# Performance work log

Measured on AMD Instinct MI355X. Metric: run time of the kernel, lower is better.

## Reference

```python
import jax, jax.numpy as jnp
import numpy as np

B, N, D, H = 2, 2048, 1024, 16
DH = D // H
SCALE = DH ** -0.5

def setup_inputs() -> dict:
    key = jax.random.key(0)
    k1, k2, k3 = jax.random.split(key, 3)
    x = jax.random.normal(k1, (B, N, D), dtype=jnp.float32)
    W_qkv = jax.random.normal(k2, (3 * D, D), dtype=jnp.float32) * (D ** -0.5)
    W_out = jax.random.normal(k3, (D, D), dtype=jnp.float32) * (D ** -0.5)
    mask = jnp.tril(jnp.ones((N, N), dtype=jnp.int32))  # causal mask; 0 -> -inf
    return {"x": x, "mask": mask, "W_qkv": W_qkv, "W_out": W_out}

def reference(x, mask, W_qkv, W_out):
    b, n, d = x.shape
    qkv = x @ W_qkv.T                                   # [B,N,3D]
    qkv = qkv.reshape(b, n, 3, H, DH).transpose(2, 0, 3, 1, 4)  # [3,B,H,N,DH]
    q, k, v = qkv[0], qkv[1], qkv[2]
    attn = jnp.einsum('bhqd,bhkd->bhqk', q, k) * SCALE  # [B,H,N,N]
    attn = jnp.where(mask == 0, -jnp.inf, attn)
    attn = jax.nn.softmax(attn, axis=-1)
    out = jnp.einsum('bhqk,bhkd->bhqd', attn, v)        # [B,H,N,DH]
    out = out.transpose(0, 2, 1, 3).reshape(b, n, d)    # [B,N,D]
    return out @ W_out.T
```

## Files before the change

### kernel.cpp

```cpp
#include <hip/hip_runtime.h>
#include <hip/hip_bf16.h>


typedef __hip_bfloat16 bf16;
typedef short bf16x8 __attribute__((ext_vector_type(8)));
typedef short bf16x4 __attribute__((ext_vector_type(4)));
typedef float f32x4 __attribute__((ext_vector_type(4)));

#define QSCALE 0.1803368801111204f

typedef __attribute__((address_space(3))) unsigned int lds_u32;
typedef const __attribute__((address_space(1))) unsigned int glob_u32;

__device__ __forceinline__ void glds16(const void* g, void* l) {
    __builtin_amdgcn_global_load_lds((glob_u32*)g, (lds_u32*)l, 16, 0, 0);
}

__device__ __forceinline__ short f2bf(float f) {
    __hip_bfloat16 h = __float2bfloat16(f);
    return *reinterpret_cast<short*>(&h);
}

__device__ __forceinline__ unsigned pack_bf16(float a, float b) {
    unsigned au = __builtin_bit_cast(unsigned, a) + 0x8000u;
    unsigned bu = __builtin_bit_cast(unsigned, b) + 0x8000u;
    return __builtin_amdgcn_perm(bu, au, 0x07060302u);
}

__global__ void cast4(const float* __restrict__ src, bf16* __restrict__ dst, int n4) {
    int i = blockIdx.x * blockDim.x + threadIdx.x;
    if (i < n4) {
        float4 f = reinterpret_cast<const float4*>(src)[i];
        short4 s;
        s.x = f2bf(f.x); s.y = f2bf(f.y); s.z = f2bf(f.z); s.w = f2bf(f.w);
        reinterpret_cast<short4*>(dst)[i] = s;
    }
}

template<int EPI>
__global__ __launch_bounds__(256)
void gemm128(const bf16* __restrict__ A, const bf16* __restrict__ Bt,
             float* __restrict__ Cf,
             bf16* __restrict__ qp, bf16* __restrict__ kp, bf16* __restrict__ vp,
             int K, int Ncols) {
    __shared__ alignas(16) short As[2][4096];
    __shared__ alignas(16) short Bs[2][4096];

    const int tid = threadIdx.x;
    const int wave = tid >> 6, lane = tid & 63;
    const int quad = lane >> 4, l16 = lane & 15;
    const int wm = wave >> 1, wn = wave & 1;
    const int m0 = blockIdx.x * 128;
    const int n0 = blockIdx.y * 128;

    f32x4 acc[4][4] = {};

    const int srow = tid >> 2;
    const int skk  = (((tid & 3) ^ ((tid >> 3) & 3))) * 8;
    const bf16* Ag = A  + (size_t)(m0 + srow) * K + skk;
    const bf16* Bg = Bt + (size_t)(n0 + srow) * K + skk;
    const size_t rowskip = (size_t)64 * K;
    short* Asl = &As[0][0] + tid * 8;
    short* Bsl = &Bs[0][0] + tid * 8;

    const int xk = (quad ^ ((l16 >> 1) & 3)) * 8;
    const int arow = wm * 64 + l16;
    const int brow = wn * 64 + l16;

    const int KI = K >> 5;
    glds16(Ag, Asl);
    glds16(Ag + rowskip, Asl + 2048);
    glds16(Bg, Bsl);
    glds16(Bg + rowskip, Bsl + 2048);
    __syncthreads();

    int buf = 0;
    for (int ki = 0; ki < KI; ++ki) {
        if (ki + 1 < KI) {
            const bf16* ag = Ag + (ki + 1) * 32;
            const bf16* bg = Bg + (ki + 1) * 32;
            short* ad = Asl + (buf ^ 1) * 4096;
            short* bd = Bsl + (buf ^ 1) * 4096;
            glds16(ag, ad);
            glds16(ag + rowskip, ad + 2048);
            glds16(bg, bd);
            glds16(bg + rowskip, bd + 2048);
        }
        const short* ab = &As[buf][0];
        const short* bb = &Bs[buf][0];
        bf16x8 af[4], bf[4];
        #pragma unroll
        for (int mt = 0; mt < 4; ++mt)
            af[mt] = *reinterpret_cast<const bf16x8*>(ab + (arow + mt * 16) * 32 + xk);
        #pragma unroll
        for (int nt = 0; nt < 4; ++nt)
            bf[nt] = *reinterpret_cast<const bf16x8*>(bb + (brow + nt * 16) * 32 + xk);
        #pragma unroll
        for (int mt = 0; mt < 4; ++mt)
            #pragma unroll
            for (int nt = 0; nt < 4; ++nt)
                acc[mt][nt] = __builtin_amdgcn_mfma_f32_16x16x32_bf16(
                    af[mt], bf[nt], acc[mt][nt], 0, 0, 0);
        __syncthreads();
        buf ^= 1;
    }

    #pragma unroll
    for (int mt = 0; mt < 4; ++mt) {
        #pragma unroll
        for (int nt = 0; nt < 4; ++nt) {
            #pragma unroll
            for (int r = 0; r < 4; ++r) {
                int gm = m0 + wm * 64 + mt * 16 + quad * 4 + r;
                int gn = n0 + wn * 64 + nt * 16 + l16;
                float val = acc[mt][nt][r];
                if (EPI == 0) {
                    int sel = gn >> 10, rem = gn & 1023;
                    int h = rem >> 6, dh = rem & 63;
                    int b = gm >> 11, nq = gm & 2047;
                    if (sel == 0) val *= QSCALE;
                    bf16* dst = (sel == 0) ? qp : ((sel == 1) ? kp : vp);
                    dst[((((size_t)b * 16 + h) * 2048) + nq) * 64 + dh] = __float2bfloat16(val);
                } else {
                    Cf[(size_t)gm * Ncols + gn] = val;
                }
            }
        }
    }
}

__global__ __launch_bounds__(256)
void flash_attn(const bf16* __restrict__ Q, const bf16* __restrict__ K,
                const bf16* __restrict__ V, bf16* __restrict__ O) {
    __shared__ alignas(16) short Ks[2][64][72];
    __shared__ alignas(16) short Vt[2][64][68];

    const int tid = threadIdx.x;
    const int wave = tid >> 6, lane = tid & 63;
    const int quad = lane >> 4, l16 = lane & 15;
    const int bh = blockIdx.x;
    const int yy = blockIdx.y;
    const int qt = (yy < 8) ? yy : (15 - (yy & 7));
    const int Q0 = qt * 128;
    const float NEG_INF = -__builtin_inff();

    const bf16* Qb = Q + (size_t)bh * 2048 * 64;
    const bf16* Kb = K + (size_t)bh * 2048 * 64;
    const bf16* Vb = V + (size_t)bh * 2048 * 64;

    const int qrowA = Q0 + wave * 16 + l16;
    const int qrowB = qrowA + 64;
    const bf16x8 qfA0 = *reinterpret_cast<const bf16x8*>(Qb + (size_t)qrowA * 64 + quad * 8);
    const bf16x8 qfA1 = *reinterpret_cast<const bf16x8*>(Qb + (size_t)qrowA * 64 + 32 + quad * 8);
    const bf16x8 qfB0 = *reinterpret_cast<const bf16x8*>(Qb + (size_t)qrowB * 64 + quad * 8);
    const bf16x8 qfB1 = *reinterpret_cast<const bf16x8*>(Qb + (size_t)qrowB * 64 + 32 + quad * 8);

    float lA = 0.f, lB = 0.f;
    f32x4 oA[4] = {}, oB[4] = {};

    const int krow = tid >> 2;
    const int kcol = (tid & 3) * 16;
    const int kb = (tid & 15) * 4;
    const int db = (tid >> 4) * 4;

    {
        bf16x8 a0 = *reinterpret_cast<const bf16x8*>(Kb + (size_t)krow * 64 + kcol);
        bf16x8 a1 = *reinterpret_cast<const bf16x8*>(Kb + (size_t)krow * 64 + kcol + 8);
        bf16x4 L0 = *reinterpret_cast<const bf16x4*>(Vb + (size_t)(kb + 0) * 64 + db);
        bf16x4 L1 = *reinterpret_cast<const bf16x4*>(Vb + (size_t)(kb + 1) * 64 + db);
        bf16x4 L2 = *reinterpret_cast<const bf16x4*>(Vb + (size_t)(kb + 2) * 64 + db);
        bf16x4 L3 = *reinterpret_cast<const bf16x4*>(Vb + (size_t)(kb + 3) * 64 + db);
        *reinterpret_cast<bf16x8*>(&Ks[0][krow][kcol]) = a0;
        *reinterpret_cast<bf16x8*>(&Ks[0][krow][kcol + 8]) = a1;
        #pragma unroll
        for (int j = 0; j < 4; ++j) {
            bf16x4 w; w[0] = L0[j]; w[1] = L1[j]; w[2] = L2[j]; w[3] = L3[j];
            *reinterpret_cast<bf16x4*>(&Vt[0][db + j][kb]) = w;
        }
    }
    __syncthreads();

    int buf = 0;
    for (int j0 = 0; j0 < Q0; j0 += 64) {
        const bf16* Kn = Kb + (size_t)(j0 + 64) * 64;
        const bf16* Vn = Vb + (size_t)(j0 + 64) * 64;
        bf16x8 nk0 = *reinterpret_cast<const bf16x8*>(Kn + (size_t)krow * 64 + kcol);
        bf16x8 nk1 = *reinterpret_cast<const bf16x8*>(Kn + (size_t)krow * 64 + kcol + 8);
        bf16x4 N0 = *reinterpret_cast<const bf16x4*>(Vn + (size_t)(kb + 0) * 64 + db);
        bf16x4 N1 = *reinterpret_cast<const bf16x4*>(Vn + (size_t)(kb + 1) * 64 + db);
        bf16x4 N2 = *reinterpret_cast<const bf16x4*>(Vn + (size_t)(kb + 2) * 64 + db);
        bf16x4 N3 = *reinterpret_cast<const bf16x4*>(Vn + (size_t)(kb + 3) * 64 + db);

        bf16x4 pkA[4], pkB[4];
        #pragma unroll
        for (int t = 0; t < 4; ++t) {
            bf16x8 k0 = *reinterpret_cast<const bf16x8*>(&Ks[buf][16 * t + l16][quad * 8]);
            bf16x8 k1 = *reinterpret_cast<const bf16x8*>(&Ks[buf][16 * t + l16][32 + quad * 8]);
            f32x4 sA = {}, sB = {};
            sA = __builtin_amdgcn_mfma_f32_16x16x32_bf16(k0, qfA0, sA, 0, 0, 0);
            sA = __builtin_amdgcn_mfma_f32_16x16x32_bf16(k1, qfA1, sA, 0, 0, 0);
            sB = __builtin_amdgcn_mfma_f32_16x16x32_bf16(k0, qfB0, sB, 0, 0, 0);
            sB = __builtin_amdgcn_mfma_f32_16x16x32_bf16(k1, qfB1, sB, 0, 0, 0);
            float a0 = __builtin_amdgcn_exp2f(sA[0]);
            float a1 = __builtin_amdgcn_exp2f(sA[1]);
            float a2 = __builtin_amdgcn_exp2f(sA[2]);
            float a3 = __builtin_amdgcn_exp2f(sA[3]);
            float b0 = __builtin_amdgcn_exp2f(sB[0]);
            float b1 = __builtin_amdgcn_exp2f(sB[1]);
            float b2 = __builtin_amdgcn_exp2f(sB[2]);
            float b3 = __builtin_amdgcn_exp2f(sB[3]);
            lA += (a0 + a1) + (a2 + a3);
            lB += (b0 + b1) + (b2 + b3);
            unsigned* pa = reinterpret_cast<unsigned*>(&pkA[t]);
            pa[0] = pack_bf16(a0, a1); pa[1] = pack_bf16(a2, a3);
            unsigned* pb = reinterpret_cast<unsigned*>(&pkB[t]);
            pb[0] = pack_bf16(b0, b1); pb[1] = pack_bf16(b2, b3);
        }

        #pragma unroll
        for (int t = 0; t < 4; ++t) {
            #pragma unroll
            for (int dt = 0; dt < 4; ++dt) {
                bf16x4 vf = *reinterpret_cast<const bf16x4*>(
                    &Vt[buf][dt * 16 + l16][t * 16 + quad * 4]);
                oA[dt] = __builtin_amdgcn_mfma_f32_16x16x16bf16_1k(vf, pkA[t], oA[dt], 0, 0, 0);
                oB[dt] = __builtin_amdgcn_mfma_f32_16x16x16bf16_1k(vf, pkB[t], oB[dt], 0, 0, 0);
            }
        }

        *reinterpret_cast<bf16x8*>(&Ks[buf ^ 1][krow][kcol]) = nk0;
        *reinterpret_cast<bf16x8*>(&Ks[buf ^ 1][krow][kcol + 8]) = nk1;
        #pragma unroll
        for (int j = 0; j < 4; ++j) {
            bf16x4 w; w[0] = N0[j]; w[1] = N1[j]; w[2] = N2[j]; w[3] = N3[j];
            *reinterpret_cast<bf16x4*>(&Vt[buf ^ 1][db + j][kb]) = w;
        }
        __syncthreads();
        buf ^= 1;
    }

    {
        const bf16* Kn = Kb + (size_t)(Q0 + 64) * 64;
        const bf16* Vn = Vb + (size_t)(Q0 + 64) * 64;
        bf16x8 nk0 = *reinterpret_cast<const bf16x8*>(Kn + (size_t)krow * 64 + kcol);
        bf16x8 nk1 = *reinterpret_cast<const bf16x8*>(Kn + (size_t)krow * 64 + kcol + 8);
        bf16x4 N0 = *reinterpret_cast<const bf16x4*>(Vn + (size_t)(kb + 0) * 64 + db);
        bf16x4 N1 = *reinterpret_cast<const bf16x4*>(Vn + (size_t)(kb + 1) * 64 + db);
        bf16x4 N2 = *reinterpret_cast<const bf16x4*>(Vn + (size_t)(kb + 2) * 64 + db);
        bf16x4 N3 = *reinterpret_cast<const bf16x4*>(Vn + (size_t)(kb + 3) * 64 + db);

        bf16x4 pkA[4], pkB[4];
        #pragma unroll
        for (int t = 0; t < 4; ++t) {
            bf16x8 k0 = *reinterpret_cast<const bf16x8*>(&Ks[buf][16 * t + l16][quad * 8]);
            bf16x8 k1 = *reinterpret_cast<const bf16x8*>(&Ks[buf][16 * t + l16][32 + quad * 8]);
            f32x4 sB = {};
            sB = __builtin_amdgcn_mfma_f32_16x16x32_bf16(k0, qfB0, sB, 0, 0, 0);
            sB = __builtin_amdgcn_mfma_f32_16x16x32_bf16(k1, qfB1, sB, 0, 0, 0);
            float b0 = __builtin_amdgcn_exp2f(sB[0]);
            float b1 = __builtin_amdgcn_exp2f(sB[1]);
            float b2 = __builtin_amdgcn_exp2f(sB[2]);
            float b3 = __builtin_amdgcn_exp2f(sB[3]);
            lB += (b0 + b1) + (b2 + b3);
            unsigned* pb = reinterpret_cast<unsigned*>(&pkB[t]);
            pb[0] = pack_bf16(b0, b1); pb[1] = pack_bf16(b2, b3);
            if (t <= wave) {
                f32x4 sA = {};
                sA = __builtin_amdgcn_mfma_f32_16x16x32_bf16(k0, qfA0, sA, 0, 0, 0);
                sA = __builtin_amdgcn_mfma_f32_16x16x32_bf16(k1, qfA1, sA, 0, 0, 0);
                if (t == wave) {
                    #pragma unroll
                    for (int r = 0; r < 4; ++r)
                        if (quad * 4 + r > l16) sA[r] = NEG_INF;
                }
                float a0 = __builtin_amdgcn_exp2f(sA[0]);
                float a1 = __builtin_amdgcn_exp2f(sA[1]);
                float a2 = __builtin_amdgcn_exp2f(sA[2]);
                float a3 = __builtin_amdgcn_exp2f(sA[3]);
                lA += (a0 + a1) + (a2 + a3);
                unsigned* pa = reinterpret_cast<unsigned*>(&pkA[t]);
                pa[0] = pack_bf16(a0, a1); pa[1] = pack_bf16(a2, a3);
            }
        }
        #pragma unroll
        for (int t = 0; t < 4; ++t) {
            #pragma unroll
            for (int dt = 0; dt < 4; ++dt) {
                bf16x4 vf = *reinterpret_cast<const bf16x4*>(
                    &Vt[buf][dt * 16 + l16][t * 16 + quad * 4]);
                oB[dt] = __builtin_amdgcn_mfma_f32_16x16x16bf16_1k(vf, pkB[t], oB[dt], 0, 0, 0);
                if (t <= wave)
                    oA[dt] = __builtin_amdgcn_mfma_f32_16x16x16bf16_1k(vf, pkA[t], oA[dt], 0, 0, 0);
            }
        }

        *reinterpret_cast<bf16x8*>(&Ks[buf ^ 1][krow][kcol]) = nk0;
        *reinterpret_cast<bf16x8*>(&Ks[buf ^ 1][krow][kcol + 8]) = nk1;
        #pragma unroll
        for (int j = 0; j < 4; ++j) {
            bf16x4 w; w[0] = N0[j]; w[1] = N1[j]; w[2] = N2[j]; w[3] = N3[j];
            *reinterpret_cast<bf16x4*>(&Vt[buf ^ 1][db + j][kb]) = w;
        }
        __syncthreads();
        buf ^= 1;
    }

    {
        bf16x4 pkB[4];
        #pragma unroll
        for (int t = 0; t < 4; ++t) {
            if (t <= wave) {
                bf16x8 k0 = *reinterpret_cast<const bf16x8*>(&Ks[buf][16 * t + l16][quad * 8]);
                bf16x8 k1 = *reinterpret_cast<const bf16x8*>(&Ks[buf][16 * t + l16][32 + quad * 8]);
                f32x4 sB = {};
                sB = __builtin_amdgcn_mfma_f32_16x16x32_bf16(k0, qfB0, sB, 0, 0, 0);
                sB = __builtin_amdgcn_mfma_f32_16x16x32_bf16(k1, qfB1, sB, 0, 0, 0);
                if (t == wave) {
                    #pragma unroll
                    for (int r = 0; r < 4; ++r)
                        if (quad * 4 + r > l16) sB[r] = NEG_INF;
                }
                float b0 = __builtin_amdgcn_exp2f(sB[0]);
                float b1 = __builtin_amdgcn_exp2f(sB[1]);
                float b2 = __builtin_amdgcn_exp2f(sB[2]);
                float b3 = __builtin_amdgcn_exp2f(sB[3]);
                lB += (b0 + b1) + (b2 + b3);
                unsigned* pb = reinterpret_cast<unsigned*>(&pkB[t]);
                pb[0] = pack_bf16(b0, b1); pb[1] = pack_bf16(b2, b3);
            }
        }
        #pragma unroll
        for (int t = 0; t < 4; ++t) {
            if (t <= wave) {
                #pragma unroll
                for (int dt = 0; dt < 4; ++dt) {
                    bf16x4 vf = *reinterpret_cast<const bf16x4*>(
                        &Vt[buf][dt * 16 + l16][t * 16 + quad * 4]);
                    oB[dt] = __builtin_amdgcn_mfma_f32_16x16x16bf16_1k(vf, pkB[t], oB[dt], 0, 0, 0);
                }
            }
        }
    }

    lA += __shfl_xor(lA, 16, 64);
    lA += __shfl_xor(lA, 32, 64);
    lB += __shfl_xor(lB, 16, 64);
    lB += __shfl_xor(lB, 32, 64);
    const float invA = 1.f / lA;
    const float invB = 1.f / lB;

    const int b = bh >> 4, h = bh & 15;
    bf16* orowA = O + ((size_t)b * 2048 + qrowA) * 1024 + h * 64;
    bf16* orowB = O + ((size_t)b * 2048 + qrowB) * 1024 + h * 64;
    #pragma unroll
    for (int dt = 0; dt < 4; ++dt) {
        bf16x4 wA, wB;
        unsigned* ua = reinterpret_cast<unsigned*>(&wA);
        ua[0] = pack_bf16(oA[dt][0] * invA, oA[dt][1] * invA);
        ua[1] = pack_bf16(oA[dt][2] * invA, oA[dt][3] * invA);
        *reinterpret_cast<bf16x4*>(orowA + dt * 16 + quad * 4) = wA;
        unsigned* ub = reinterpret_cast<unsigned*>(&wB);
        ub[0] = pack_bf16(oB[dt][0] * invB, oB[dt][1] * invB);
        ub[1] = pack_bf16(oB[dt][2] * invB, oB[dt][3] * invB);
        *reinterpret_cast<bf16x4*>(orowB + dt * 16 + quad * 4) = wB;
    }
}

extern "C" void kernel_launch(void* const* d_in, const int* in_sizes, int n_in,
                              void* d_out, int out_size, void* d_ws, size_t ws_size,
                              hipStream_t stream) {
    const float* x    = (const float*)d_in[0];
    const float* Wqkv = (const float*)d_in[2];
    const float* Wout = (const float*)d_in[3];
    float* out = (float*)d_out;

    char* ws = (char*)d_ws;
    bf16* x_bf    = (bf16*)(ws);
    bf16* wqkv_bf = (bf16*)(ws + 8388608);
    bf16* wout_bf = (bf16*)(ws + 14680064);
    bf16* q       = (bf16*)(ws + 16777216);
    bf16* k       = (bf16*)(ws + 25165824);
    bf16* v       = (bf16*)(ws + 33554432);
    bf16* ao      = (bf16*)(ws + 41943040);

    cast4<<<4096, 256, 0, stream>>>(x, x_bf, 1048576);
    cast4<<<3072, 256, 0, stream>>>(Wqkv, wqkv_bf, 786432);
    cast4<<<1024, 256, 0, stream>>>(Wout, wout_bf, 262144);

    gemm128<0><<<dim3(32, 24), 256, 0, stream>>>(x_bf, wqkv_bf, nullptr, q, k, v, 1024, 3072);
    flash_attn<<<dim3(32, 16), 256, 0, stream>>>(q, k, v, ao);
    gemm128<1><<<dim3(32, 8), 256, 0, stream>>>(ao, wout_bf, out, nullptr, nullptr, nullptr, 1024, 1024);
}
```

Baseline: 180.6 us.

## Use 256x256 tiled 8-wave QKV GEMM and fuse input casts into one launch

Replaces the 128x128 QKV projection GEMM with a 256x256-tile, 512-thread kernel. It double-buffers LDS through direct global-to-LDS loads with XOR swizzling, and interleaves four MFMA quarter-blocks with staged loads, barriers and priority hints. The three cast kernels are merged into one launch. The larger tile raises data reuse per load but gives only 192 blocks, which may underfill the CUs. It also uses 128 KB of LDS per block and carries a tricky hand-written wait-count schedule.

After: 188.7 us. 1.05x slower.

```diff
diff --git a/kernel.cpp b/kernel.cpp
--- a/kernel.cpp
+++ b/kernel.cpp
@@ -27,13 +27,173 @@
     return __builtin_amdgcn_perm(bu, au, 0x07060302u);
 }
 
-__global__ void cast4(const float* __restrict__ src, bf16* __restrict__ dst, int n4) {
+__global__ void cast_all(const float* __restrict__ x, const float* __restrict__ wqkv,
+                         const float* __restrict__ wout,
+                         bf16* __restrict__ xb, bf16* __restrict__ wqkvb,
+                         bf16* __restrict__ woutb) {
     int i = blockIdx.x * blockDim.x + threadIdx.x;
-    if (i < n4) {
-        float4 f = reinterpret_cast<const float4*>(src)[i];
-        short4 s;
-        s.x = f2bf(f.x); s.y = f2bf(f.y); s.z = f2bf(f.z); s.w = f2bf(f.w);
-        reinterpret_cast<short4*>(dst)[i] = s;
+    const float4* s; short4* d; int o;
+    if (i < 1048576)            { s = (const float4*)x;    d = (short4*)xb;    o = i; }
+    else if (i < 1048576 + 786432) { s = (const float4*)wqkv; d = (short4*)wqkvb; o = i - 1048576; }
+    else                        { s = (const float4*)wout; d = (short4*)woutb; o = i - 1834848 + 32; }
+    if (i >= 1048576 + 786432) o = i - 1835008;
+    float4 f = s[o];
+    short4 v;
+    v.x = f2bf(f.x); v.y = f2bf(f.y); v.z = f2bf(f.z); v.w = f2bf(f.w);
+    d[o] = v;
+}
+
+#define MMAC(mh, nh) do {                                                          \
+    _Pragma("unroll")                                                              \
+    for (int mt = 0; mt < 4; ++mt) {                                               \
+        _Pragma("unroll")                                                          \
+        for (int j = 0; j < 2; ++j) {                                              \
+            f32x4 c = acc[(mh)*4+mt][(nh)*2+j];                                    \
+            c = __builtin_amdgcn_mfma_f32_16x16x32_bf16(af[mt][0], bfr[nh][j][0], c, 0, 0, 0); \
+            c = __builtin_amdgcn_mfma_f32_16x16x32_bf16(af[mt][1], bfr[nh][j][1], c, 0, 0, 0); \
+            acc[(mh)*4+mt][(nh)*2+j] = c;                                          \
+        }                                                                          \
+    }                                                                              \
+} while (0)
+
+__global__ __launch_bounds__(512, 2)
+void gemm256_qkv(const bf16* __restrict__ A, const bf16* __restrict__ Bt,
+                 bf16* __restrict__ qp, bf16* __restrict__ kp, bf16* __restrict__ vp) {
+    constexpr int K = 1024, NT = K / 64;
+    __shared__ alignas(16) short As[2 * 16384];
+    __shared__ alignas(16) short Bs[2 * 16384];
+
+    const int tid  = threadIdx.x;
+    const int lane = tid & 63;
+    const int wave = tid >> 6;
+    const int quad = lane >> 4, l16 = lane & 15;
+    const int wm = wave >> 2;
+    const int wn = wave & 3;
+    const int hb = wn >> 1;
+    const int m0 = blockIdx.x * 256;
+    const int n0 = blockIdx.y * 256;
+
+    const int ts    = tid ^ (((tid >> 5) & 1) << 1) ^ (((tid >> 6) & 1) << 2);
+    const int tsrow = ts >> 3;
+    const int tscol = (ts & 7) * 8;
+
+    const bf16* Ag = A  + (size_t)(m0 + tsrow) * K + tscol;
+    const bf16* Bg = Bt + (size_t)(n0 + tsrow) * K + tscol;
+    short* Asl = As + tid * 8;
+    short* Bsl = Bs + tid * 8;
+
+    auto stageA = [&](int T, int h) {
+        short* d = Asl + (T & 1) * 16384 + h * 8192;
+        const bf16* g = Ag + (size_t)(h * 128) * K + T * 64;
+        glds16(g, d);
+        glds16(g + (size_t)64 * K, d + 4096);
+    };
+    auto stageB = [&](int T, int h) {
+        short* d = Bsl + (T & 1) * 16384 + h * 8192;
+        const bf16* g = Bg + (size_t)(h * 128) * K + T * 64;
+        glds16(g, d);
+        glds16(g + (size_t)64 * K, d + 4096);
+    };
+
+    bf16x8 af[4][2];
+    bf16x8 bfr[2][2][2];
+    f32x4  acc[8][4] = {};
+
+    auto rdA = [&](const char* ab, int mh) {
+        #pragma unroll
+        for (int mt = 0; mt < 4; ++mt) {
+            const int lr = mh * 64 + mt * 16 + l16;
+            #pragma unroll
+            for (int ks = 0; ks < 2; ++ks) {
+                int o = lr * 128 + ks * 64 + quad * 16;
+                o ^= (((o >> 9) & 1) << 5) ^ (((o >> 10) & 1) << 6);
+                af[mt][ks] = *reinterpret_cast<const bf16x8*>(ab + o);
+            }
+        }
+    };
+    auto rdB = [&](const char* bb, int nh) {
+        #pragma unroll
+        for (int j = 0; j < 2; ++j) {
+            const int lr = (wn & 1) * 64 + (nh * 2 + j) * 16 + l16;
+            #pragma unroll
+            for (int ks = 0; ks < 2; ++ks) {
+                int o = lr * 128 + ks * 64 + quad * 16;
+                o ^= (((o >> 9) & 1) << 5) ^ (((o >> 10) & 1) << 6);
+                bfr[nh][j][ks] = *reinterpret_cast<const bf16x8*>(bb + o);
+            }
+        }
+    };
+
+    stageA(0, 0); stageA(0, 1); stageB(0, 0); stageB(0, 1);
+    stageB(1, 0); stageA(1, 0);
+    asm volatile("s_waitcnt vmcnt(4)" ::: "memory");
+    __builtin_amdgcn_s_barrier();
+
+    for (int T = 0; T < NT; ++T) {
+        const char* ab = (const char*)As + (T & 1) * 32768 + wm * 16384;
+        const char* bb = (const char*)Bs + (T & 1) * 32768 + hb * 16384;
+        const bool st1 = (T + 1 < NT), st2 = (T + 2 < NT);
+
+        rdA(ab, 0);
+        rdB(bb, 0);
+        if (st1) stageB(T + 1, 1);
+        __builtin_amdgcn_s_barrier();
+        asm volatile("s_waitcnt lgkmcnt(0)" ::: "memory");
+        __builtin_amdgcn_sched_barrier(0);
+        __builtin_amdgcn_s_setprio(1);
+        MMAC(0, 0);
+        __builtin_amdgcn_s_setprio(0);
+        __builtin_amdgcn_s_barrier();
+
+        rdB(bb, 1);
+        if (st1) stageA(T + 1, 1);
+        __builtin_amdgcn_s_barrier();
+        asm volatile("s_waitcnt lgkmcnt(0)" ::: "memory");
+        __builtin_amdgcn_sched_barrier(0);
+        __builtin_amdgcn_s_setprio(1);
+        MMAC(0, 1);
+        __builtin_amdgcn_s_setprio(0);
+        __builtin_amdgcn_s_barrier();
+
+        rdA(ab, 1);
+        if (st2) stageB(T + 2, 0);
+        __builtin_amdgcn_s_barrier();
+        asm volatile("s_waitcnt lgkmcnt(0)" ::: "memory");
+        __builtin_amdgcn_sched_barrier(0);
+        __builtin_amdgcn_s_setprio(1);
+        MMAC(1, 1);
+        __builtin_amdgcn_s_setprio(0);
+        __builtin_amdgcn_s_barrier();
+
+        if (st2) stageA(T + 2, 0);
+        __builtin_amdgcn_s_setprio(1);
+        MMAC(1, 0);
+        __builtin_amdgcn_s_setprio(0);
+        if (st1) {
+            if (st2) asm volatile("s_waitcnt vmcnt(4)" ::: "memory");
+            else     asm volatile("s_waitcnt vmcnt(0)" ::: "memory");
+            __builtin_amdgcn_s_barrier();
+        }
+    }
+
+    const int sel  = n0 >> 10;
+    const int remb = n0 & 1023;
+    bf16* dst = (sel == 0) ? qp : ((sel == 1) ? kp : vp);
+    const float scale = (sel == 0) ? QSCALE : 1.0f;
+    #pragma unroll
+    for (int mt = 0; mt < 8; ++mt) {
+        #pragma unroll
+        for (int nt = 0; nt < 4; ++nt) {
+            #pragma unroll
+            for (int r = 0; r < 4; ++r) {
+                int gm  = m0 + wm * 128 + mt * 16 + quad * 4 + r;
+                int rem = remb + wn * 64 + nt * 16 + l16;
+                int h = rem >> 6, dh = rem & 63;
+                int b = gm >> 11, nq = gm & 2047;
+                dst[((((size_t)b * 16 + h) * 2048) + nq) * 64 + dh] =
+                    __float2bfloat16(acc[mt][nt][r] * scale);
+            }
+        }
     }
 }
 
@@ -383,11 +543,8 @@
     bf16* v       = (bf16*)(ws + 33554432);
     bf16* ao      = (bf16*)(ws + 41943040);
 
-    cast4<<<4096, 256, 0, stream>>>(x, x_bf, 1048576);
-    cast4<<<3072, 256, 0, stream>>>(Wqkv, wqkv_bf, 786432);
-    cast4<<<1024, 256, 0, stream>>>(Wout, wout_bf, 262144);
-
-    gemm128<0><<<dim3(32, 24), 256, 0, stream>>>(x_bf, wqkv_bf, nullptr, q, k, v, 1024, 3072);
+    cast_all<<<8192, 256, 0, stream>>>(x, Wqkv, Wout, x_bf, wqkv_bf, wout_bf);
+    gemm256_qkv<<<dim3(16, 12), 512, 0, stream>>>(x_bf, wqkv_bf, q, k, v);
     flash_attn<<<dim3(32, 16), 256, 0, stream>>>(q, k, v, ao);
     gemm128<1><<<dim3(32, 8), 256, 0, stream>>>(ao, wout_bf, out, nullptr, nullptr, nullptr, 1024, 1024);
 }
```
